# Performance work log

Measured on AMD Instinct MI355X. Metric: run time of the kernel, lower is better.

## Reference

```python
import jax, jax.numpy as jnp
import numpy as np

B, S, HID, H, DK = 2, 2048, 1024, 16, 64
SCALE = DK ** -0.5
NEG = -1000000000.0


def setup_inputs() -> dict:
    key = jax.random.key(0)
    ks = jax.random.split(key, 14)
    std = HID ** -0.5
    return {
        "q": jax.random.normal(ks[0], (B, S, HID), jnp.float32),
        "k": jax.random.normal(ks[1], (B, S, HID), jnp.float32),
        "v": jax.random.normal(ks[2], (B, S, HID), jnp.float32),
        "attn_bias": jax.random.normal(ks[3], (B, H, S, S), jnp.float32),
        "mask": jax.random.randint(ks[4], (B, S), 0, 2, jnp.int32),
        "Wq": jax.random.normal(ks[5], (HID, H * DK), jnp.float32) * std,
        "bq": jnp.zeros((H * DK,), jnp.float32),
        "Wk": jax.random.normal(ks[6], (HID, H * DK), jnp.float32) * std,
        "bk": jnp.zeros((H * DK,), jnp.float32),
        "Wv": jax.random.normal(ks[7], (HID, H * DK), jnp.float32) * std,
        "bv": jnp.zeros((H * DK,), jnp.float32),
        "Wo": jax.random.normal(ks[8], (H * DK, H * DK), jnp.float32) * std,
        "bo": jnp.zeros((H * DK,), jnp.float32),
    }


def reference(q, k, v, attn_bias, mask, Wq, bq, Wk, bk, Wv, bv, Wo, bo):
    Bq = q.shape[0]
    # projections -> [B, H, S, DK]
    qh = (q @ Wq + bq).reshape(Bq, -1, H, DK).transpose(0, 2, 1, 3) * SCALE
    kh = (k @ Wk + bk).reshape(Bq, -1, H, DK).transpose(0, 2, 1, 3)
    vh = (v @ Wv + bv).reshape(Bq, -1, H, DK).transpose(0, 2, 1, 3)
    # scores [B, H, Sq, Sk]
    scores = jnp.einsum("bhqd,bhkd->bhqk", qh, kh)
    k_mask = mask[:, None, None, :]  # [B,1,1,Sk]
    scores = jnp.where(k_mask == 0, NEG, scores)
    scores = scores + attn_bias
    attn = jax.nn.softmax(scores, axis=-1)  # dropout rate 0.0 -> identity
    x = jnp.einsum("bhqk,bhkd->bhqd", attn, vh)
    x = x * mask[:, None, :, None].astype(x.dtype)  # zero masked query rows
    x = x.transpose(0, 2, 1, 3).reshape(Bq, -1, H * DK)
    return x @ Wo + bo
```

## Files before the change

### kernel.cpp

```cpp
#include <hip/hip_runtime.h>


typedef __bf16 bf16x8 __attribute__((ext_vector_type(8)));
typedef float f32x4 __attribute__((ext_vector_type(4)));
typedef unsigned short u16x8 __attribute__((ext_vector_type(8)));

#define NEGV (-1000000000.0f)

typedef __attribute__((address_space(3))) unsigned int lds_u32;
typedef const __attribute__((address_space(1))) unsigned int glb_u32;

static __device__ __forceinline__ void async16(const void* g, void* l) {
  __builtin_amdgcn_global_load_lds((glb_u32*)g, (lds_u32*)l, 16, 0, 0);
}

static __device__ __forceinline__ unsigned short f2b(float f) {
  unsigned int u = __float_as_uint(f);
  return (unsigned short)((u + 0x7FFFu + ((u >> 16) & 1u)) >> 16);
}

static __device__ __forceinline__ bf16x8 ld8(const unsigned short* p) {
  return __builtin_bit_cast(bf16x8, *(const u16x8*)p);
}

__global__ __launch_bounds__(256) void k_cvt(const float* __restrict__ A0, const float* __restrict__ A1,
                                             const float* __restrict__ A2,
                                             unsigned short* __restrict__ O0, unsigned short* __restrict__ O1,
                                             unsigned short* __restrict__ O2) {
  const float* A = (blockIdx.z == 0) ? A0 : (blockIdx.z == 1) ? A1 : A2;
  unsigned short* O = (blockIdx.z == 0) ? O0 : (blockIdx.z == 1) ? O1 : O2;
  size_t i = ((size_t)blockIdx.x * 256 + threadIdx.x) * 8;
  float4 f0 = *(const float4*)(A + i);
  float4 f1 = *(const float4*)(A + i + 4);
  u16x8 h;
  h[0] = f2b(f0.x); h[1] = f2b(f0.y); h[2] = f2b(f0.z); h[3] = f2b(f0.w);
  h[4] = f2b(f1.x); h[5] = f2b(f1.y); h[6] = f2b(f1.z); h[7] = f2b(f1.w);
  *(u16x8*)(O + i) = h;
}

__global__ __launch_bounds__(256) void k_wtrans(const float* __restrict__ W0, const float* __restrict__ W1,
                                                const float* __restrict__ W2, const float* __restrict__ W3,
                                                unsigned short* __restrict__ T0, unsigned short* __restrict__ T1,
                                                unsigned short* __restrict__ T2, unsigned short* __restrict__ T3) {
  const float* W = (blockIdx.z == 0) ? W0 : (blockIdx.z == 1) ? W1 : (blockIdx.z == 2) ? W2 : W3;
  unsigned short* Wt = (blockIdx.z == 0) ? T0 : (blockIdx.z == 1) ? T1 : (blockIdx.z == 2) ? T2 : T3;
  __shared__ float tile[32][33];
  int k0 = blockIdx.x * 32, n0 = blockIdx.y * 32;
  int tx = threadIdx.x, ty = threadIdx.y;
  #pragma unroll
  for (int i = 0; i < 32; i += 8)
    tile[ty + i][tx] = W[(size_t)(k0 + ty + i) * 1024 + n0 + tx];
  __syncthreads();
  #pragma unroll
  for (int i = 0; i < 32; i += 8)
    Wt[(size_t)(n0 + ty + i) * 1024 + k0 + tx] = f2b(tile[tx][ty + i]);
}

__global__ __launch_bounds__(256) void k_gemm_qkv(
    const unsigned short* __restrict__ A0, const unsigned short* __restrict__ A1,
    const unsigned short* __restrict__ A2,
    const unsigned short* __restrict__ W0, const unsigned short* __restrict__ W1,
    const unsigned short* __restrict__ W2,
    const float* __restrict__ b0, const float* __restrict__ b1, const float* __restrict__ b2,
    unsigned short* __restrict__ o0, unsigned short* __restrict__ o1, unsigned short* __restrict__ o2) {
  int f = blockIdx.x;
  int mode = f >> 8;
  int r = f & 255;
  int m0 = (r & 31) * 128, n0 = (r >> 5) * 128;
  const unsigned short* Ab = (mode == 0) ? A0 : (mode == 1) ? A1 : A2;
  const unsigned short* Bt = (mode == 0) ? W0 : (mode == 1) ? W1 : W2;
  const float* bias = (mode == 0) ? b0 : (mode == 1) ? b1 : b2;
  unsigned short* outb = (mode == 0) ? o0 : (mode == 1) ? o1 : o2;

  __shared__ __align__(16) unsigned short smem[128 * 136];
  unsigned short* As = smem;
  unsigned short* Bs = smem + 128 * 64;
  int t = threadIdx.x;
  int wave = t >> 6, lane = t & 63;
  int r16 = lane & 15, quad = lane >> 4;
  int wm = (wave >> 1) * 64, wn = (wave & 1) * 64;
  f32x4 acc[4][4] = {};

  for (int k0 = 0; k0 < 1024; k0 += 64) {
    __syncthreads();
    #pragma unroll
    for (int i = 0; i < 4; i++) {
      int row = wave * 32 + i * 8 + (lane >> 3);
      int sw = (((lane & 7) ^ (row & 7))) * 8;
      async16(Ab + (size_t)(m0 + row) * 1024 + k0 + sw, &As[(wave * 32 + i * 8) * 64]);
      async16(Bt + (size_t)(n0 + row) * 1024 + k0 + sw, &Bs[(wave * 32 + i * 8) * 64]);
    }
    __syncthreads();
    #pragma unroll
    for (int kk2 = 0; kk2 < 2; kk2++) {
      bf16x8 av[4], bv[4];
      int gq = quad + kk2 * 4;
      #pragma unroll
      for (int mt = 0; mt < 4; mt++) {
        int lm = wm + mt * 16 + r16;
        av[mt] = ld8(&As[lm * 64 + (gq ^ (lm & 7)) * 8]);
      }
      #pragma unroll
      for (int nt = 0; nt < 4; nt++) {
        int ln = wn + nt * 16 + r16;
        bv[nt] = ld8(&Bs[ln * 64 + (gq ^ (ln & 7)) * 8]);
      }
      #pragma unroll
      for (int mt = 0; mt < 4; mt++)
        #pragma unroll
        for (int nt = 0; nt < 4; nt++)
          acc[mt][nt] = __builtin_amdgcn_mfma_f32_16x16x32_bf16(av[mt], bv[nt], acc[mt][nt], 0, 0, 0);
    }
  }

  __syncthreads();
  float scale = (mode == 0) ? 0.125f : 1.0f;
  #pragma unroll
  for (int nt = 0; nt < 4; nt++) {
    int ln = wn + nt * 16 + r16;
    float bv = bias[n0 + ln];
    #pragma unroll
    for (int mt = 0; mt < 4; mt++)
      #pragma unroll
      for (int rr = 0; rr < 4; rr++) {
        int lm = wm + mt * 16 + quad * 4 + rr;
        unsigned short hv = f2b((acc[mt][nt][rr] + bv) * scale);
        if (mode == 2) smem[ln * 136 + lm] = hv;
        else           smem[lm * 136 + ln] = hv;
      }
  }
  __syncthreads();
  int rrow = t >> 1, half = t & 1;
  const unsigned short* src = smem + rrow * 136 + half * 64;
  if (mode == 2) {
    int b = m0 >> 11, s0 = m0 & 2047;
    int gn = n0 + rrow, h = gn >> 6, d = gn & 63;
    unsigned short* dst = outb + ((size_t)(b * 16 + h) * 64 + d) * 2048 + s0 + half * 64;
    #pragma unroll
    for (int j = 0; j < 8; j++) *(int4*)(dst + j * 8) = *(const int4*)(src + j * 8);
  } else {
    int gm = m0 + rrow, b = gm >> 11, s = gm & 2047;
    int h = (n0 + half * 64) >> 6;
    unsigned short* dst = outb + ((size_t)(b * 16 + h) * 2048 + s) * 64;
    #pragma unroll
    for (int j = 0; j < 8; j++) *(int4*)(dst + j * 8) = *(const int4*)(src + j * 8);
  }
}

__global__ __launch_bounds__(256) void k_gemm_o(const unsigned short* __restrict__ Ab,
                                                const unsigned short* __restrict__ Bt,
                                                const float* __restrict__ bias,
                                                float* __restrict__ outf) {
  __shared__ __align__(16) unsigned short As[64 * 64];
  __shared__ __align__(16) unsigned short Bs[128 * 64];
  int t = threadIdx.x;
  int wave = t >> 6, lane = t & 63;
  int r16 = lane & 15, quad = lane >> 4;
  int f = blockIdx.x;
  int m0 = (f & 63) * 64, n0 = (f >> 6) * 128;
  int wm = (wave & 1) * 32, wn = (wave >> 1) * 64;
  f32x4 acc[2][4] = {};

  for (int k0 = 0; k0 < 1024; k0 += 64) {
    __syncthreads();
    #pragma unroll
    for (int i = 0; i < 2; i++) {
      int row = wave * 16 + i * 8 + (lane >> 3);
      int sw = (((lane & 7) ^ (row & 7))) * 8;
      async16(Ab + (size_t)(m0 + row) * 1024 + k0 + sw, &As[(wave * 16 + i * 8) * 64]);
    }
    #pragma unroll
    for (int i = 0; i < 4; i++) {
      int row = wave * 32 + i * 8 + (lane >> 3);
      int sw = (((lane & 7) ^ (row & 7))) * 8;
      async16(Bt + (size_t)(n0 + row) * 1024 + k0 + sw, &Bs[(wave * 32 + i * 8) * 64]);
    }
    __syncthreads();
    #pragma unroll
    for (int kk2 = 0; kk2 < 2; kk2++) {
      int gq = quad + kk2 * 4;
      bf16x8 av[2], bv[4];
      #pragma unroll
      for (int mt = 0; mt < 2; mt++) {
        int lm = wm + mt * 16 + r16;
        av[mt] = ld8(&As[lm * 64 + (gq ^ (lm & 7)) * 8]);
      }
      #pragma unroll
      for (int nt = 0; nt < 4; nt++) {
        int ln = wn + nt * 16 + r16;
        bv[nt] = ld8(&Bs[ln * 64 + (gq ^ (ln & 7)) * 8]);
      }
      #pragma unroll
      for (int mt = 0; mt < 2; mt++)
        #pragma unroll
        for (int nt = 0; nt < 4; nt++)
          acc[mt][nt] = __builtin_amdgcn_mfma_f32_16x16x32_bf16(av[mt], bv[nt], acc[mt][nt], 0, 0, 0);
    }
  }
  #pragma unroll
  for (int nt = 0; nt < 4; nt++) {
    int gn = n0 + wn + nt * 16 + r16;
    float bv = bias[gn];
    #pragma unroll
    for (int mt = 0; mt < 2; mt++)
      #pragma unroll
      for (int rr = 0; rr < 4; rr++) {
        int gm = m0 + wm + mt * 16 + quad * 4 + rr;
        outf[(size_t)gm * 1024 + gn] = acc[mt][nt][rr] + bv;
      }
  }
}

__global__ __launch_bounds__(256) void k_attn(const unsigned short* __restrict__ qh,
                                              const unsigned short* __restrict__ kh,
                                              const unsigned short* __restrict__ vt,
                                              const float* __restrict__ bias,
                                              const int* __restrict__ mask,
                                              unsigned short* __restrict__ xb) {
  __shared__ __align__(16) unsigned short Ks[64 * 64];
  __shared__ __align__(16) unsigned short Vs[64 * 64];
  __shared__ __align__(16) unsigned short Ps[128 * 72];
  __shared__ float kmb[64];
  int t = threadIdx.x;
  int wave = t >> 6, lane = t & 63;
  int r16 = lane & 15, quad = lane >> 4, quad8 = quad * 8;
  int w32 = wave * 32;
  int f = blockIdx.x;
  int bh = f & 31, q0 = (f >> 5) * 128;
  int b = bh >> 4, h = bh & 15;
  const unsigned short* kbase = kh + (size_t)bh * 2048 * 64;
  const unsigned short* vbase = vt + (size_t)bh * 64 * 2048;
  const float* bbase = bias + (size_t)bh * 2048 * 2048 + (size_t)q0 * 2048;

  bf16x8 qf[2][2];
  #pragma unroll
  for (int mt = 0; mt < 2; mt++) {
    const unsigned short* qrow = qh + (size_t)bh * 2048 * 64 + (size_t)(q0 + w32 + mt * 16 + r16) * 64;
    qf[mt][0] = ld8(qrow + quad8);
    qf[mt][1] = ld8(qrow + 32 + quad8);
  }
  const u16x8 onesu = {0x3F80, 0x3F80, 0x3F80, 0x3F80, 0x3F80, 0x3F80, 0x3F80, 0x3F80};
  const bf16x8 ones = __builtin_bit_cast(bf16x8, onesu);

  f32x4 o[2][4] = {};
  f32x4 accl[2] = {};
  float mrow[2][4] = {{-1e38f, -1e38f, -1e38f, -1e38f}, {-1e38f, -1e38f, -1e38f, -1e38f}};

  float bpf[2][4][4];
  #pragma unroll
  for (int mt = 0; mt < 2; mt++)
    #pragma unroll
    for (int nt = 0; nt < 4; nt++)
      #pragma unroll
      for (int rr = 0; rr < 4; rr++)
        bpf[mt][nt][rr] = bbase[(size_t)(w32 + mt * 16 + quad * 4 + rr) * 2048 + nt * 16 + r16];

  for (int k0 = 0; k0 < 2048; k0 += 64) {
    __syncthreads();
    #pragma unroll
    for (int j = 0; j < 2; j++) {
      int row = wave * 16 + j * 8 + (lane >> 3);
      int sw = (((lane & 7) ^ (row & 7))) * 8;
      async16(kbase + (size_t)(k0 + row) * 64 + sw, &Ks[(wave * 16 + j * 8) * 64]);
      async16(vbase + (size_t)row * 2048 + k0 + sw, &Vs[(wave * 16 + j * 8) * 64]);
    }
    if (t < 64) kmb[t] = (mask[b * 2048 + k0 + t] == 0) ? 1.0f : 0.0f;
    __syncthreads();

    f32x4 sc[2][4] = {};
    #pragma unroll
    for (int kk2 = 0; kk2 < 2; kk2++) {
      bf16x8 kf[4];
      int gq = quad + kk2 * 4;
      #pragma unroll
      for (int nt = 0; nt < 4; nt++) {
        int ln = nt * 16 + r16;
        kf[nt] = ld8(&Ks[ln * 64 + (gq ^ (ln & 7)) * 8]);
      }
      #pragma unroll
      for (int mt = 0; mt < 2; mt++)
        #pragma unroll
        for (int nt = 0; nt < 4; nt++)
          sc[mt][nt] = __builtin_amdgcn_mfma_f32_16x16x32_bf16(qf[mt][kk2], kf[nt], sc[mt][nt], 0, 0, 0);
    }
    #pragma unroll
    for (int mt = 0; mt < 2; mt++)
      #pragma unroll
      for (int nt = 0; nt < 4; nt++) {
        float km = kmb[nt * 16 + r16];
        #pragma unroll
        for (int rr = 0; rr < 4; rr++)
          sc[mt][nt][rr] = ((km > 0.5f) ? NEGV : sc[mt][nt][rr]) + bpf[mt][nt][rr];
      }
    {
      int kn = (k0 + 64) & 2047;
      #pragma unroll
      for (int mt = 0; mt < 2; mt++)
        #pragma unroll
        for (int nt = 0; nt < 4; nt++)
          #pragma unroll
          for (int rr = 0; rr < 4; rr++)
            bpf[mt][nt][rr] = bbase[(size_t)(w32 + mt * 16 + quad * 4 + rr) * 2048 + kn + nt * 16 + r16];
    }
    float arow[2][4];
    #pragma unroll
    for (int mt = 0; mt < 2; mt++)
      #pragma unroll
      for (int rr = 0; rr < 4; rr++) {
        float mx = fmaxf(fmaxf(sc[mt][0][rr], sc[mt][1][rr]), fmaxf(sc[mt][2][rr], sc[mt][3][rr]));
        #pragma unroll
        for (int off = 1; off < 16; off <<= 1) mx = fmaxf(mx, __shfl_xor(mx, off));
        float mn = fmaxf(mrow[mt][rr], mx);
        arow[mt][rr] = __expf(mrow[mt][rr] - mn);
        mrow[mt][rr] = mn;
        #pragma unroll
        for (int nt = 0; nt < 4; nt++) sc[mt][nt][rr] = __expf(sc[mt][nt][rr] - mn);
      }
    #pragma unroll
    for (int mt = 0; mt < 2; mt++)
      #pragma unroll
      for (int nt = 0; nt < 4; nt++)
        #pragma unroll
        for (int rr = 0; rr < 4; rr++)
          Ps[(w32 + mt * 16 + quad * 4 + rr) * 72 + nt * 16 + r16] = f2b(sc[mt][nt][rr]);
    #pragma unroll
    for (int mt = 0; mt < 2; mt++)
      #pragma unroll
      for (int rr = 0; rr < 4; rr++) {
        accl[mt][rr] *= arow[mt][rr];
        #pragma unroll
        for (int nt = 0; nt < 4; nt++) o[mt][nt][rr] *= arow[mt][rr];
      }
    #pragma unroll
    for (int kk2 = 0; kk2 < 2; kk2++) {
      bf16x8 vf[4];
      int gq = quad + kk2 * 4;
      #pragma unroll
      for (int nt = 0; nt < 4; nt++) {
        int ln = nt * 16 + r16;
        vf[nt] = ld8(&Vs[ln * 64 + (gq ^ (ln & 7)) * 8]);
      }
      #pragma unroll
      for (int mt = 0; mt < 2; mt++) {
        bf16x8 a = ld8(&Ps[(w32 + mt * 16 + r16) * 72 + kk2 * 32 + quad8]);
        accl[mt] = __builtin_amdgcn_mfma_f32_16x16x32_bf16(a, ones, accl[mt], 0, 0, 0);
        #pragma unroll
        for (int nt = 0; nt < 4; nt++)
          o[mt][nt] = __builtin_amdgcn_mfma_f32_16x16x32_bf16(a, vf[nt], o[mt][nt], 0, 0, 0);
      }
    }
  }

  #pragma unroll
  for (int mt = 0; mt < 2; mt++) {
    float inv[4];
    #pragma unroll
    for (int rr = 0; rr < 4; rr++) {
      int gq = q0 + w32 + mt * 16 + quad * 4 + rr;
      float qm = (mask[b * 2048 + gq] != 0) ? 1.0f : 0.0f;
      inv[rr] = qm / accl[mt][rr];
    }
    #pragma unroll
    for (int nt = 0; nt < 4; nt++)
      #pragma unroll
      for (int rr = 0; rr < 4; rr++) {
        int gq = q0 + w32 + mt * 16 + quad * 4 + rr;
        xb[(size_t)(b * 2048 + gq) * 1024 + h * 64 + nt * 16 + r16] = f2b(o[mt][nt][rr] * inv[rr]);
      }
  }
}

extern "C" void kernel_launch(void* const* d_in, const int* in_sizes, int n_in,
                              void* d_out, int out_size, void* d_ws, size_t ws_size,
                              hipStream_t stream) {
  const float* q = (const float*)d_in[0];
  const float* k = (const float*)d_in[1];
  const float* v = (const float*)d_in[2];
  const float* attn_bias = (const float*)d_in[3];
  const int* mask = (const int*)d_in[4];
  const float* Wq = (const float*)d_in[5];
  const float* bq = (const float*)d_in[6];
  const float* Wk = (const float*)d_in[7];
  const float* bk = (const float*)d_in[8];
  const float* Wv = (const float*)d_in[9];
  const float* bv = (const float*)d_in[10];
  const float* Wo = (const float*)d_in[11];
  const float* bo = (const float*)d_in[12];

  char* ws = (char*)d_ws;
  const size_t MB = 1u << 20;
  unsigned short* Wqt = (unsigned short*)(ws + 0 * MB);
  unsigned short* Wkt = (unsigned short*)(ws + 2 * MB);
  unsigned short* Wvt = (unsigned short*)(ws + 4 * MB);
  unsigned short* Wot = (unsigned short*)(ws + 6 * MB);
  unsigned short* qhb = (unsigned short*)(ws + 8 * MB);
  unsigned short* khb = (unsigned short*)(ws + 16 * MB);
  unsigned short* vtb = (unsigned short*)(ws + 24 * MB);
  unsigned short* xbb = (unsigned short*)(ws + 32 * MB);
  unsigned short* qcb = (unsigned short*)(ws + 40 * MB);
  unsigned short* kcb = (unsigned short*)(ws + 48 * MB);
  unsigned short* vcb = (unsigned short*)(ws + 56 * MB);

  k_cvt<<<dim3(2048, 1, 3), 256, 0, stream>>>(q, k, v, qcb, kcb, vcb);

  k_wtrans<<<dim3(32, 32, 4), dim3(32, 8), 0, stream>>>(Wq, Wk, Wv, Wo, Wqt, Wkt, Wvt, Wot);

  k_gemm_qkv<<<768, 256, 0, stream>>>(qcb, kcb, vcb, Wqt, Wkt, Wvt, bq, bk, bv,
                                      qhb, khb, vtb);

  k_attn<<<512, 256, 0, stream>>>(qhb, khb, vtb, attn_bias, mask, xbb);

  k_gemm_o<<<512, 256, 0, stream>>>(xbb, Wot, bo, (float*)d_out);
}
```

Baseline: 869.5 us.

## Compact unmasked query rows and skip masked ones; double-buffer K/V tiles

New measurement: 815.8 us. 6.2% less time.

```diff
diff --git a/kernel.cpp b/kernel.cpp
--- a/kernel.cpp
+++ b/kernel.cpp
@@ -36,6 +36,37 @@
   h[0] = f2b(f0.x); h[1] = f2b(f0.y); h[2] = f2b(f0.z); h[3] = f2b(f0.w);
   h[4] = f2b(f1.x); h[5] = f2b(f1.y); h[6] = f2b(f1.z); h[7] = f2b(f1.w);
   *(u16x8*)(O + i) = h;
+}
+
+__global__ __launch_bounds__(256) void k_zero(unsigned short* __restrict__ p) {
+  size_t i = ((size_t)blockIdx.x * 256 + threadIdx.x) * 8;
+  u16x8 z = {0, 0, 0, 0, 0, 0, 0, 0};
+  *(u16x8*)(p + i) = z;
+}
+
+__global__ __launch_bounds__(64) void k_scan(const int* __restrict__ mask,
+                                             int* __restrict__ idx, int* __restrict__ cnt) {
+  int b = blockIdx.x;
+  int t = threadIdx.x;
+  int m[32];
+  int c = 0;
+  #pragma unroll
+  for (int j = 0; j < 32; j++) {
+    m[j] = (mask[b * 2048 + t * 32 + j] != 0) ? 1 : 0;
+    c += m[j];
+  }
+  int inc = c;
+  #pragma unroll
+  for (int off = 1; off < 64; off <<= 1) {
+    int v = __shfl_up(inc, off);
+    if (t >= off) inc += v;
+  }
+  int pos = inc - c;
+  #pragma unroll
+  for (int j = 0; j < 32; j++) {
+    if (m[j]) { idx[b * 2048 + pos] = t * 32 + j; pos++; }
+  }
+  if (t == 63) cnt[b] = inc;
 }
 
 __global__ __launch_bounds__(256) void k_wtrans(const float* __restrict__ W0, const float* __restrict__ W1,
@@ -216,26 +247,61 @@
                                               const unsigned short* __restrict__ vt,
                                               const float* __restrict__ bias,
                                               const int* __restrict__ mask,
+                                              const int* __restrict__ idx,
+                                              const int* __restrict__ cnt,
                                               unsigned short* __restrict__ xb) {
-  __shared__ __align__(16) unsigned short Ks[64 * 64];
-  __shared__ __align__(16) unsigned short Vs[64 * 64];
+  __shared__ __align__(16) unsigned short Ks[2][64 * 64];
+  __shared__ __align__(16) unsigned short Vs[2][64 * 64];
   __shared__ __align__(16) unsigned short Ps[128 * 72];
-  __shared__ float kmb[64];
+  __shared__ float kmb[2][64];
+  __shared__ int idxL[128];
   int t = threadIdx.x;
   int wave = t >> 6, lane = t & 63;
   int r16 = lane & 15, quad = lane >> 4, quad8 = quad * 8;
   int w32 = wave * 32;
   int f = blockIdx.x;
-  int bh = f & 31, q0 = (f >> 5) * 128;
+  int bh = f & 31, qt = f >> 5;
   int b = bh >> 4, h = bh & 15;
+  int cb = cnt[b];
+  int q0 = qt * 128;
+  if (q0 >= cb) return;
+
+  if (t < 128) idxL[t] = (q0 + t < cb) ? idx[b * 2048 + q0 + t] : idx[b * 2048];
   const unsigned short* kbase = kh + (size_t)bh * 2048 * 64;
   const unsigned short* vbase = vt + (size_t)bh * 64 * 2048;
-  const float* bbase = bias + (size_t)bh * 2048 * 2048 + (size_t)q0 * 2048;
-
+
+#define STAGE_KV(bufi, kt_) do {                                                     \
+    int k0s = (kt_) * 64;                                                            \
+    _Pragma("unroll")                                                                \
+    for (int j = 0; j < 2; j++) {                                                    \
+      int row = wave * 16 + j * 8 + (lane >> 3);                                     \
+      int sw = (((lane & 7) ^ (row & 7))) * 8;                                       \
+      async16(kbase + (size_t)(k0s + row) * 64 + sw, &Ks[bufi][(wave * 16 + j * 8) * 64]); \
+      async16(vbase + (size_t)row * 2048 + k0s + sw, &Vs[bufi][(wave * 16 + j * 8) * 64]); \
+    }                                                                                \
+    if (t < 64) kmb[bufi][t] = (mask[b * 2048 + k0s + t] == 0) ? 1.0f : 0.0f;        \
+  } while (0)
+
+  STAGE_KV(0, 0);
+  __syncthreads();
+
+  int sm[2][4];
+  int vm[2][4];
+  int boff[2][4];
+  #pragma unroll
+  for (int mt = 0; mt < 2; mt++)
+    #pragma unroll
+    for (int rr = 0; rr < 4; rr++) {
+      int j = w32 + mt * 16 + quad * 4 + rr;
+      sm[mt][rr] = idxL[j];
+      vm[mt][rr] = (q0 + j) < cb;
+      boff[mt][rr] = (bh * 2048 + sm[mt][rr]) * 2048;
+    }
   bf16x8 qf[2][2];
   #pragma unroll
   for (int mt = 0; mt < 2; mt++) {
-    const unsigned short* qrow = qh + (size_t)bh * 2048 * 64 + (size_t)(q0 + w32 + mt * 16 + r16) * 64;
+    int sqr = idxL[w32 + mt * 16 + r16];
+    const unsigned short* qrow = qh + ((size_t)bh * 2048 + sqr) * 64;
     qf[mt][0] = ld8(qrow + quad8);
     qf[mt][1] = ld8(qrow + 32 + quad8);
   }
@@ -253,19 +319,11 @@
     for (int nt = 0; nt < 4; nt++)
       #pragma unroll
       for (int rr = 0; rr < 4; rr++)
-        bpf[mt][nt][rr] = bbase[(size_t)(w32 + mt * 16 + quad * 4 + rr) * 2048 + nt * 16 + r16];
-
-  for (int k0 = 0; k0 < 2048; k0 += 64) {
-    __syncthreads();
-    #pragma unroll
-    for (int j = 0; j < 2; j++) {
-      int row = wave * 16 + j * 8 + (lane >> 3);
-      int sw = (((lane & 7) ^ (row & 7))) * 8;
-      async16(kbase + (size_t)(k0 + row) * 64 + sw, &Ks[(wave * 16 + j * 8) * 64]);
-      async16(vbase + (size_t)row * 2048 + k0 + sw, &Vs[(wave * 16 + j * 8) * 64]);
-    }
-    if (t < 64) kmb[t] = (mask[b * 2048 + k0 + t] == 0) ? 1.0f : 0.0f;
-    __syncthreads();
+        bpf[mt][nt][rr] = bias[(size_t)(unsigned)boff[mt][rr] + nt * 16 + r16];
+
+  int cur = 0;
+  for (int kt = 0; kt < 32; kt++) {
+    if (kt < 31) STAGE_KV(cur ^ 1, kt + 1);
 
     f32x4 sc[2][4] = {};
     #pragma unroll
@@ -275,7 +333,7 @@
       #pragma unroll
       for (int nt = 0; nt < 4; nt++) {
         int ln = nt * 16 + r16;
-        kf[nt] = ld8(&Ks[ln * 64 + (gq ^ (ln & 7)) * 8]);
+        kf[nt] = ld8(&Ks[cur][ln * 64 + (gq ^ (ln & 7)) * 8]);
       }
       #pragma unroll
       for (int mt = 0; mt < 2; mt++)
@@ -287,20 +345,20 @@
     for (int mt = 0; mt < 2; mt++)
       #pragma unroll
       for (int nt = 0; nt < 4; nt++) {
-        float km = kmb[nt * 16 + r16];
+        float km = kmb[cur][nt * 16 + r16];
         #pragma unroll
         for (int rr = 0; rr < 4; rr++)
           sc[mt][nt][rr] = ((km > 0.5f) ? NEGV : sc[mt][nt][rr]) + bpf[mt][nt][rr];
       }
     {
-      int kn = (k0 + 64) & 2047;
+      int kn = ((kt + 1) & 31) * 64;
       #pragma unroll
       for (int mt = 0; mt < 2; mt++)
         #pragma unroll
         for (int nt = 0; nt < 4; nt++)
           #pragma unroll
           for (int rr = 0; rr < 4; rr++)
-            bpf[mt][nt][rr] = bbase[(size_t)(w32 + mt * 16 + quad * 4 + rr) * 2048 + kn + nt * 16 + r16];
+            bpf[mt][nt][rr] = bias[(size_t)(unsigned)boff[mt][rr] + kn + nt * 16 + r16];
     }
     float arow[2][4];
     #pragma unroll
@@ -338,7 +396,7 @@
       #pragma unroll
       for (int nt = 0; nt < 4; nt++) {
         int ln = nt * 16 + r16;
-        vf[nt] = ld8(&Vs[ln * 64 + (gq ^ (ln & 7)) * 8]);
+        vf[nt] = ld8(&Vs[cur][ln * 64 + (gq ^ (ln & 7)) * 8]);
       }
       #pragma unroll
       for (int mt = 0; mt < 2; mt++) {
@@ -349,25 +407,22 @@
           o[mt][nt] = __builtin_amdgcn_mfma_f32_16x16x32_bf16(a, vf[nt], o[mt][nt], 0, 0, 0);
       }
     }
-  }
-
-  #pragma unroll
-  for (int mt = 0; mt < 2; mt++) {
-    float inv[4];
+    __syncthreads();
+    cur ^= 1;
+  }
+
+  #pragma unroll
+  for (int mt = 0; mt < 2; mt++)
     #pragma unroll
     for (int rr = 0; rr < 4; rr++) {
-      int gq = q0 + w32 + mt * 16 + quad * 4 + rr;
-      float qm = (mask[b * 2048 + gq] != 0) ? 1.0f : 0.0f;
-      inv[rr] = qm / accl[mt][rr];
-    }
-    #pragma unroll
-    for (int nt = 0; nt < 4; nt++)
-      #pragma unroll
-      for (int rr = 0; rr < 4; rr++) {
-        int gq = q0 + w32 + mt * 16 + quad * 4 + rr;
-        xb[(size_t)(b * 2048 + gq) * 1024 + h * 64 + nt * 16 + r16] = f2b(o[mt][nt][rr] * inv[rr]);
-      }
-  }
+      if (!vm[mt][rr]) continue;
+      float iv = 1.0f / accl[mt][rr];
+      size_t base = ((size_t)(b * 2048 + sm[mt][rr])) * 1024 + h * 64;
+      #pragma unroll
+      for (int nt = 0; nt < 4; nt++)
+        xb[base + nt * 16 + r16] = f2b(o[mt][nt][rr] * iv);
+    }
+#undef STAGE_KV
 }
 
 extern "C" void kernel_launch(void* const* d_in, const int* in_sizes, int n_in,
@@ -400,6 +455,8 @@
   unsigned short* qcb = (unsigned short*)(ws + 40 * MB);
   unsigned short* kcb = (unsigned short*)(ws + 48 * MB);
   unsigned short* vcb = (unsigned short*)(ws + 56 * MB);
+  int* idxb = (int*)(ws + 40 * MB);
+  int* cntb = (int*)(ws + 40 * MB + 16384);
 
   k_cvt<<<dim3(2048, 1, 3), 256, 0, stream>>>(q, k, v, qcb, kcb, vcb);
 
@@ -408,7 +465,11 @@
   k_gemm_qkv<<<768, 256, 0, stream>>>(qcb, kcb, vcb, Wqt, Wkt, Wvt, bq, bk, bv,
                                       qhb, khb, vtb);
 
-  k_attn<<<512, 256, 0, stream>>>(qhb, khb, vtb, attn_bias, mask, xbb);
+  k_scan<<<2, 64, 0, stream>>>(mask, idxb, cntb);
+
+  k_zero<<<2048, 256, 0, stream>>>(xbb);
+
+  k_attn<<<512, 256, 0, stream>>>(qhb, khb, vtb, attn_bias, mask, idxb, cntb, xbb);
 
   k_gemm_o<<<512, 256, 0, stream>>>(xbb, Wot, bo, (float*)d_out);
 }
```
